# Performance work log

Hardware: AMD Instinct MI355X
Metric: run time of the kernel (lower is better)

Reference implementation:

```python
import jax, jax.numpy as jnp
import numpy as np

N_NODES = 100000
N_GRAPHS = 64

def gcn_conv(x, edge_index, W, b, num_nodes):
    # PyG GCNConv: x' = D^-1/2 (A + I) D^-1/2 (x W) + b
    h = x @ W  # [N, out]
    row, col = edge_index[0], edge_index[1]
    loops = jnp.arange(num_nodes, dtype=row.dtype)
    src = jnp.concatenate([row, loops])  # message source (x_j)
    dst = jnp.concatenate([col, loops])  # aggregation target
    deg = jax.ops.segment_sum(jnp.ones_like(src, dtype=h.dtype), dst,
                              num_segments=num_nodes)
    dinv = jnp.where(deg > 0, jax.lax.rsqrt(deg), 0.0)
    norm = dinv[src] * dinv[dst]  # [E+N]
    msgs = h[src] * norm[:, None]  # gather-transform
    out = jax.ops.segment_sum(msgs, dst, num_segments=num_nodes)  # scatter
    return out + b

def global_mean_pool(x, batch, num_graphs):
    sums = jax.ops.segment_sum(x, batch, num_segments=num_graphs)
    cnts = jax.ops.segment_sum(jnp.ones((x.shape[0],), x.dtype), batch,
                               num_segments=num_graphs)
    return sums / jnp.maximum(cnts, 1.0)[:, None]

def setup_inputs() -> dict:
    key = jax.random.key(0)
    ks = jax.random.split(key, 12)
    d_in, d_hid, d_mid, d_out = 128, 128, 20, 10
    n_edges = 1600000
    x = jax.random.normal(ks[0], (N_NODES, d_in), dtype=jnp.float32)
    edge_index = jax.random.randint(ks[1], (2, n_edges), 0, N_NODES, dtype=jnp.int64)
    batch = jnp.sort(jax.random.randint(ks[2], (N_NODES,), 0, N_GRAPHS, dtype=jnp.int64))
    def glorot(k, fan_in, fan_out):
        s = (6.0 / (fan_in + fan_out)) ** 0.5
        return jax.random.uniform(k, (fan_in, fan_out), jnp.float32, -s, s)
    return {
        "x": x, "edge_index": edge_index, "batch": batch,
        "W1": glorot(ks[3], d_in, d_hid), "b1": jnp.zeros((d_hid,), jnp.float32),
        "W2": glorot(ks[4], d_hid, d_hid), "b2": jnp.zeros((d_hid,), jnp.float32),
        "fc1_W": glorot(ks[5], d_hid, d_mid), "fc1_b": jnp.zeros((d_mid,), jnp.float32),
        "fc2_W": glorot(ks[6], d_mid, d_out), "fc2_b": jnp.zeros((d_out,), jnp.float32),
    }

def reference(x, edge_index, batch, W1, b1, W2, b2, fc1_W, fc1_b, fc2_W, fc2_b):
    # eval mode: dropout is identity
    h = gcn_conv(x, edge_index, W1, b1, N_NODES)
    h = jax.nn.elu(h)
    h = gcn_conv(h, edge_index, W2, b2, N_NODES)
    g = global_mean_pool(h, batch, N_GRAPHS)  # [G, hidden]
    g = jax.nn.relu(g @ fc1_W + fc1_b)
    g = g @ fc2_W + fc2_b
    return jax.nn.log_softmax(g, axis=1)
```

## Files before the change

kernel.cpp:

```cpp
#include <hip/hip_runtime.h>
#include <math.h>

#define DH 128
#define BCAP 16384

typedef __bf16 bf8_t __attribute__((ext_vector_type(8)));
typedef short short8 __attribute__((ext_vector_type(8)));
typedef float f4_t __attribute__((ext_vector_type(4)));
typedef float f2_t __attribute__((ext_vector_type(2)));

__device__ inline unsigned short f2b(float f) {
    unsigned int u = __builtin_bit_cast(unsigned int, f);
    u = u + 0x7fffu + ((u >> 16) & 1u);
    return (unsigned short)(u >> 16);
}
__device__ inline float b2f(unsigned short h) {
    return __builtin_bit_cast(float, (unsigned int)h << 16);
}

__global__ __launch_bounds__(256) void k_bucket(const int* __restrict__ row,
                                                const int* __restrict__ col,
                                                int E, int nbuck, int chunk,
                                                unsigned int* __restrict__ pairs,
                                                int* __restrict__ bcur) {
    __shared__ int lcnt[256];
    __shared__ int lbase[256];
    __shared__ unsigned int srec[8192];
    int t = threadIdx.x;
    int e0 = blockIdx.x * chunk;
    int e1 = min(e0 + chunk, E);
    lcnt[t] = 0;
    __syncthreads();
    for (int i = e0 + t; i < e1; i += 256) {
        int d = col[i];
        int b = d >> 9;
        int slot = atomicAdd(&lcnt[b], 1);
        srec[i - e0] = ((unsigned int)b << 22) | ((unsigned int)(d & 511) << 13)
                     | (unsigned int)slot;
    }
    __syncthreads();
    if (t < nbuck) {
        int c = lcnt[t];
        lbase[t] = (c > 0) ? atomicAdd(&bcur[t * 16], c) : 0;
    }
    __syncthreads();
    for (int i = e0 + t; i < e1; i += 256) {
        unsigned int r = srec[i - e0];
        int b = r >> 22;
        unsigned int dl = (r >> 13) & 511u;
        int slot = (int)(r & 8191u);
        int g = lbase[b] + slot;
        if (g < BCAP)
            pairs[(size_t)b * BCAP + g] = ((unsigned int)row[i] << 9) | dl;
    }
}

__global__ __launch_bounds__(256) void k_build(const unsigned int* __restrict__ pairs,
                                               const int* __restrict__ bcur,
                                               int nbuck, int N,
                                               int* __restrict__ off,
                                               int* __restrict__ dpd,
                                               float* __restrict__ dinv,
                                               int* __restrict__ csr) {
    __shared__ int cnt2[512];
    __shared__ int pd2[512];
    __shared__ int excl[512];
    __shared__ int curi[512];
    __shared__ int stmp[256];
    int b = blockIdx.x, t = threadIdx.x;
    int cnt = min(bcur[b * 16], BCAP);
    int base = b * BCAP;
    int node0 = b << 9;
    int nodes = min(512, N - node0);
    cnt2[t] = (t < nodes) ? 1 : 0;
    cnt2[t + 256] = (t + 256 < nodes) ? 1 : 0;
    __syncthreads();
    const unsigned int* pp = pairs + (size_t)b * BCAP;
    for (int i = t; i < cnt; i += 256)
        atomicAdd(&cnt2[pp[i] & 511u], 1);
    __syncthreads();
    pd2[t] = (cnt2[t] + 15) & ~15;
    pd2[t + 256] = (cnt2[t + 256] + 15) & ~15;
    __syncthreads();
    stmp[t] = pd2[2 * t] + pd2[2 * t + 1];
    __syncthreads();
    for (int d = 1; d < 256; d <<= 1) {
        int v = (t >= d) ? stmp[t - d] : 0;
        __syncthreads();
        stmp[t] += v;
        __syncthreads();
    }
    int pre = (t == 0) ? 0 : stmp[t - 1];
    excl[2 * t] = pre;
    excl[2 * t + 1] = pre + pd2[2 * t];
    __syncthreads();
    for (int n = t; n < 512; n += 256) {
        int avail = BCAP - excl[n];
        int pdc = pd2[n];
        if (pdc > avail) pdc = (avail > 0) ? (avail & ~15) : 0;
        pd2[n] = pdc;
    }
    __syncthreads();
    if (t < nodes) {
        off[node0 + t] = base + excl[t];
        dpd[node0 + t] = pd2[t];
        dinv[node0 + t] = rsqrtf((float)cnt2[t]);
    }
    int t2 = t + 256;
    if (t2 < nodes) {
        off[node0 + t2] = base + excl[t2];
        dpd[node0 + t2] = pd2[t2];
        dinv[node0 + t2] = rsqrtf((float)cnt2[t2]);
    }
    curi[t] = excl[t] + 1; curi[t + 256] = excl[t + 256] + 1;
    __syncthreads();
    for (int n = t; n < nodes; n += 256)
        if (excl[n] < BCAP) csr[base + excl[n]] = node0 + n;
    for (int i = t; i < cnt; i += 256) {
        unsigned int p = pp[i];
        int d = (int)(p & 511u);
        int slot = atomicAdd(&curi[d], 1);
        if (slot < BCAP) csr[base + slot] = (int)(p >> 9);
    }
    for (int n = t; n < 512; n += 256) {
        int e0 = excl[n] + cnt2[n];
        int e1 = excl[n] + pd2[n];
        for (int k = e0; k < e1; k++) csr[base + k] = N;
    }
}

__global__ void k_prepW(const float* __restrict__ W1, const float* __restrict__ W2,
                        unsigned short* __restrict__ Wt1, unsigned short* __restrict__ Wt2,
                        unsigned int* __restrict__ t8zrow) {
    int t = blockIdx.x * blockDim.x + threadIdx.x;
    if (blockIdx.x == 0 && threadIdx.x < 32) t8zrow[threadIdx.x] = 0u;
    int v = t & 16383;
    int k = v >> 7, n = v & 127;
    if (t < 16384) {
        Wt1[n * DH + k] = f2b(W1[k * DH + n]);
    } else {
        int p = ((k & 15) << 3) | (k >> 4);
        Wt2[n * DH + p] = f2b(W2[k * DH + n]);
    }
}

__global__ __launch_bounds__(256) void k_gemm_mfma(const void* __restrict__ Xin, int x_is_bf16,
                                                   const unsigned short* __restrict__ Wt,
                                                   const float* __restrict__ dinv,
                                                   unsigned char* __restrict__ Y, int nrows) {
    __shared__ unsigned short Xs[64 * 136];
    __shared__ unsigned short Ws[128 * 136];
    int t = threadIdx.x;
    int row0 = blockIdx.x * 64;

    for (int v = t; v < 128 * 32; v += 256) {
        int n = v >> 5, kq = v & 31;
        ushort4 w = ((const ushort4*)Wt)[v];
        *(ushort4*)&Ws[n * 136 + kq * 4] = w;
    }
    if (x_is_bf16) {
        const unsigned short* X = (const unsigned short*)Xin;
        for (int v = t; v < 64 * 32; v += 256) {
            int r = v >> 5, cq = v & 31;
            int gr = row0 + r;
            ushort4 h;
            if (gr < nrows) h = ((const ushort4*)X)[(size_t)gr * 32 + cq];
            else { h.x = 0; h.y = 0; h.z = 0; h.w = 0; }
            *(ushort4*)&Xs[r * 136 + cq * 4] = h;
        }
    } else {
        const float* X = (const float*)Xin;
        for (int v = t; v < 64 * 32; v += 256) {
            int r = v >> 5, cq = v & 31;
            int gr = row0 + r;
            ushort4 h;
            if (gr < nrows) {
                float4 xv = ((const float4*)X)[(size_t)gr * 32 + cq];
                h.x = f2b(xv.x); h.y = f2b(xv.y); h.z = f2b(xv.z); h.w = f2b(xv.w);
            } else { h.x = 0; h.y = 0; h.z = 0; h.w = 0; }
            *(ushort4*)&Xs[r * 136 + cq * 4] = h;
        }
    }
    __syncthreads();

    int w = t >> 6;
    int lane = t & 63;
    int quad = lane >> 4;
    int l16 = lane & 15;
    int rw = w * 16;

    f4_t acc[8];
#pragma unroll
    for (int j = 0; j < 8; j++) acc[j] = (f4_t){0.f, 0.f, 0.f, 0.f};

#pragma unroll
    for (int kk = 0; kk < 4; kk++) {
        int k0 = kk * 32;
        bf8_t a = __builtin_bit_cast(bf8_t,
            *(const short8*)&Xs[(rw + l16) * 136 + k0 + quad * 8]);
#pragma unroll
        for (int j = 0; j < 8; j++) {
            bf8_t b = __builtin_bit_cast(bf8_t,
                *(const short8*)&Ws[(j * 16 + l16) * 136 + k0 + quad * 8]);
            acc[j] = __builtin_amdgcn_mfma_f32_16x16x32_bf16(a, b, acc[j], 0, 0, 0);
        }
    }

#pragma unroll
    for (int reg = 0; reg < 4; reg++) {
        int r = row0 + rw + quad * 4 + reg;
        if (r < nrows) {
            float dv = dinv[r];
            float v0 = acc[0][reg] * dv, v1 = acc[1][reg] * dv;
            float v2 = acc[2][reg] * dv, v3 = acc[3][reg] * dv;
            float v4 = acc[4][reg] * dv, v5 = acc[5][reg] * dv;
            float v6 = acc[6][reg] * dv, v7 = acc[7][reg] * dv;
            int d0 = __builtin_amdgcn_cvt_pk_fp8_f32(v0, v1, 0, false);
            d0 = __builtin_amdgcn_cvt_pk_fp8_f32(v2, v3, d0, true);
            int d1 = __builtin_amdgcn_cvt_pk_fp8_f32(v4, v5, 0, false);
            d1 = __builtin_amdgcn_cvt_pk_fp8_f32(v6, v7, d1, true);
            *(uint2*)&Y[(size_t)r * DH + l16 * 8] = make_uint2((unsigned)d0, (unsigned)d1);
        }
    }
}

#define AGG_ROUND(IDX)                                                     \
    {                                                                      \
        int ea = be + i;                                                   \
        unsigned v0 = ((unsigned)IDX(ea)     << 7) | l5b;                  \
        unsigned v1 = ((unsigned)IDX(ea + 1) << 7) | l5b;                  \
        unsigned v2 = ((unsigned)IDX(ea + 2) << 7) | l5b;                  \
        unsigned v3 = ((unsigned)IDX(ea + 3) << 7) | l5b;                  \
        unsigned v4 = ((unsigned)IDX(ea + 4) << 7) | l5b;                  \
        unsigned v5 = ((unsigned)IDX(ea + 5) << 7) | l5b;                  \
        unsigned v6 = ((unsigned)IDX(ea + 6) << 7) | l5b;                  \
        unsigned v7 = ((unsigned)IDX(ea + 7) << 7) | l5b;                  \
        unsigned int u0 = *(const unsigned int*)(Tb + v0);                 \
        unsigned int u1 = *(const unsigned int*)(Tb + v1);                 \
        unsigned int u2 = *(const unsigned int*)(Tb + v2);                 \
        unsigned int u3 = *(const unsigned int*)(Tb + v3);                 \
        unsigned int u4 = *(const unsigned int*)(Tb + v4);                 \
        unsigned int u5 = *(const unsigned int*)(Tb + v5);                 \
        unsigned int u6 = *(const unsigned int*)(Tb + v6);                 \
        unsigned int u7 = *(const unsigned int*)(Tb + v7);                 \
        accA01 += __builtin_amdgcn_cvt_pk_f32_fp8(u0, false);              \
        accA23 += __builtin_amdgcn_cvt_pk_f32_fp8(u0, true);               \
        accB01 += __builtin_amdgcn_cvt_pk_f32_fp8(u1, false);              \
        accB23 += __builtin_amdgcn_cvt_pk_f32_fp8(u1, true);               \
        accA01 += __builtin_amdgcn_cvt_pk_f32_fp8(u2, false);              \
        accA23 += __builtin_amdgcn_cvt_pk_f32_fp8(u2, true);               \
        accB01 += __builtin_amdgcn_cvt_pk_f32_fp8(u3, false);              \
        accB23 += __builtin_amdgcn_cvt_pk_f32_fp8(u3, true);               \
        accA01 += __builtin_amdgcn_cvt_pk_f32_fp8(u4, false);              \
        accA23 += __builtin_amdgcn_cvt_pk_f32_fp8(u4, true);               \
        accB01 += __builtin_amdgcn_cvt_pk_f32_fp8(u5, false);              \
        accB23 += __builtin_amdgcn_cvt_pk_f32_fp8(u5, true);               \
        accA01 += __builtin_amdgcn_cvt_pk_f32_fp8(u6, false);              \
        accA23 += __builtin_amdgcn_cvt_pk_f32_fp8(u6, true);               \
        accB01 += __builtin_amdgcn_cvt_pk_f32_fp8(u7, false);              \
        accB23 += __builtin_amdgcn_cvt_pk_f32_fp8(u7, true);               \
    }

__global__ __launch_bounds__(256) void k_agg(const unsigned char* __restrict__ T,
                                             unsigned short* __restrict__ Out,
                                             const float* __restrict__ dinv,
                                             const int* __restrict__ off,
                                             const int* __restrict__ dpd,
                                             const int* __restrict__ csr,
                                             const float* __restrict__ bias,
                                             int N) {
    __shared__ int ofs[16];
    __shared__ int pds[16];
    __shared__ float dv16[16];
    __shared__ int sidx[768];
    int t = threadIdx.x;
    int d0 = blockIdx.x * 16;
    if (t < 16) {
        int n = min(d0 + t, N - 1);
        ofs[t] = off[n];
        pds[t] = dpd[n];
        dv16[t] = dinv[n];
    }
    __syncthreads();
    int s0 = ofs[0];
    int span = ofs[15] + pds[15] - s0;
    int scnt = min(span, 768);
    for (int k = t; k < scnt; k += 256) sidx[k] = csr[s0 + k];
    __syncthreads();

    int w = t >> 6;
    int lane = t & 63;
    int half = lane >> 5;
    int l5 = lane & 31;
    unsigned l5b = (unsigned)(l5 << 2);
    const char* Tb = (const char*)T;

    int c0 = ((l5 & 1) << 6) | (l5 >> 1);
    float bb0 = bias[c0], bb1 = bias[c0 + 16], bb2 = bias[c0 + 32], bb3 = bias[c0 + 48];

    for (int ni = 0; ni < 4; ni++) {
        int nl = 4 * w + ni;
        int nd = d0 + nl;
        if (nd >= N) break;
        int eL = ofs[nl] - s0;
        int pd = pds[nl];
        int K = pd >> 1;
        int be = eL + half * K;

        f2_t accA01 = (f2_t){0.f, 0.f}, accA23 = (f2_t){0.f, 0.f};
        f2_t accB01 = (f2_t){0.f, 0.f}, accB23 = (f2_t){0.f, 0.f};

        if (eL + pd <= scnt) {
#define IDX_L(e) sidx[e]
            for (int i = 0; i < K; i += 8) AGG_ROUND(IDX_L)
#undef IDX_L
        } else {
            const int* gp = csr + s0;
#define IDX_G(e) gp[e]
            for (int i = 0; i < K; i += 8) AGG_ROUND(IDX_G)
#undef IDX_G
        }

        float a0 = accA01[0] + accB01[0];
        float a1 = accA01[1] + accB01[1];
        float a2 = accA23[0] + accB23[0];
        float a3 = accA23[1] + accB23[1];
        a0 += __shfl_xor(a0, 32);
        a1 += __shfl_xor(a1, 32);
        a2 += __shfl_xor(a2, 32);
        a3 += __shfl_xor(a3, 32);

        if (!half) {
            float dv = dv16[nl];
            float o0 = a0 * dv + bb0;
            float o1 = a1 * dv + bb1;
            float o2 = a2 * dv + bb2;
            float o3 = a3 * dv + bb3;
            o0 = o0 > 0.f ? o0 : __expf(o0) - 1.f;
            o1 = o1 > 0.f ? o1 : __expf(o1) - 1.f;
            o2 = o2 > 0.f ? o2 : __expf(o2) - 1.f;
            o3 = o3 > 0.f ? o3 : __expf(o3) - 1.f;
            unsigned int p0 = (unsigned int)f2b(o0) | ((unsigned int)f2b(o1) << 16);
            unsigned int p1 = (unsigned int)f2b(o2) | ((unsigned int)f2b(o3) << 16);
            *(uint2*)&Out[(size_t)nd * DH + (l5 << 2)] = make_uint2(p0, p1);
        }
    }
}

__global__ __launch_bounds__(256) void k_aggp(const unsigned char* __restrict__ T,
                                              float* __restrict__ Gsum,
                                              const float* __restrict__ dinv,
                                              const int* __restrict__ off,
                                              const int* __restrict__ dpd,
                                              const int* __restrict__ csr,
                                              const float* __restrict__ bias,
                                              const int* __restrict__ batch,
                                              int N) {
    __shared__ int ofs[16];
    __shared__ int pds[16];
    __shared__ float dv16[16];
    __shared__ int gfs[16];
    __shared__ int sidx[768];
    __shared__ float Gacc[16 * DH];
    int t = threadIdx.x;
    int d0 = blockIdx.x * 16;
    if (t < 16) {
        int n = min(d0 + t, N - 1);
        ofs[t] = off[n];
        pds[t] = dpd[n];
        dv16[t] = dinv[n];
        gfs[t] = batch[n];
    }
    for (int k = t; k < 16 * DH; k += 256) Gacc[k] = 0.f;
    __syncthreads();
    int s0 = ofs[0];
    int g0 = gfs[0];
    int span = ofs[15] + pds[15] - s0;
    int scnt = min(span, 768);
    for (int k = t; k < scnt; k += 256) sidx[k] = csr[s0 + k];
    __syncthreads();

    int w = t >> 6;
    int lane = t & 63;
    int half = lane >> 5;
    int l5 = lane & 31;
    unsigned l5b = (unsigned)(l5 << 2);
    const char* Tb = (const char*)T;

    int c0 = ((l5 & 1) << 6) | (l5 >> 1);
    float bb0 = bias[c0], bb1 = bias[c0 + 16], bb2 = bias[c0 + 32], bb3 = bias[c0 + 48];

    for (int ni = 0; ni < 4; ni++) {
        int nl = 4 * w + ni;
        int nd = d0 + nl;
        if (nd >= N) break;
        int eL = ofs[nl] - s0;
        int pd = pds[nl];
        int K = pd >> 1;
        int be = eL + half * K;

        f2_t accA01 = (f2_t){0.f, 0.f}, accA23 = (f2_t){0.f, 0.f};
        f2_t accB01 = (f2_t){0.f, 0.f}, accB23 = (f2_t){0.f, 0.f};

        if (eL + pd <= scnt) {
#define IDX_L(e) sidx[e]
            for (int i = 0; i < K; i += 8) AGG_ROUND(IDX_L)
#undef IDX_L
        } else {
            const int* gp = csr + s0;
#define IDX_G(e) gp[e]
            for (int i = 0; i < K; i += 8) AGG_ROUND(IDX_G)
#undef IDX_G
        }

        float a0 = accA01[0] + accB01[0];
        float a1 = accA01[1] + accB01[1];
        float a2 = accA23[0] + accB23[0];
        float a3 = accA23[1] + accB23[1];
        a0 += __shfl_xor(a0, 32);
        a1 += __shfl_xor(a1, 32);
        a2 += __shfl_xor(a2, 32);
        a3 += __shfl_xor(a3, 32);

        if (!half) {
            float dv = dv16[nl];
            int sbase = (gfs[nl] - g0) * DH;
            atomicAdd(&Gacc[sbase + c0],      a0 * dv + bb0);
            atomicAdd(&Gacc[sbase + c0 + 16], a1 * dv + bb1);
            atomicAdd(&Gacc[sbase + c0 + 32], a2 * dv + bb2);
            atomicAdd(&Gacc[sbase + c0 + 48], a3 * dv + bb3);
        }
    }
    __syncthreads();
    int nspan = gfs[15] - g0 + 1;
    for (int k = t; k < nspan * DH; k += 256) {
        float v = Gacc[k];
        if (v != 0.f) atomicAdd(&Gsum[(size_t)(g0 + (k >> 7)) * DH + (k & 127)], v);
    }
}

__global__ __launch_bounds__(64) void k_head(const float* __restrict__ Gsum,
                                             const int* __restrict__ batch, int N,
                                             const float* __restrict__ W1,
                                             const float* __restrict__ b1,
                                             const float* __restrict__ W2,
                                             const float* __restrict__ b2,
                                             float* __restrict__ out) {
    int g = blockIdx.x;
    int t = threadIdx.x;
    __shared__ float gv[DH];
    __shared__ float mid[20];
    __shared__ float o[10];
    int lo = 0, hi = N;
    while (lo < hi) { int m = (lo + hi) >> 1; if (batch[m] < g) lo = m + 1; else hi = m; }
    int s = lo;
    hi = N;
    while (lo < hi) { int m = (lo + hi) >> 1; if (batch[m] < g + 1) lo = m + 1; else hi = m; }
    float inv = 1.f / fmaxf((float)(lo - s), 1.f);
    for (int i = t; i < DH; i += 64) gv[i] = Gsum[g * DH + i] * inv;
    __syncthreads();
    if (t < 20) {
        float a = b1[t];
        for (int k = 0; k < DH; k++) a += gv[k] * W1[k * 20 + t];
        mid[t] = fmaxf(a, 0.f);
    }
    __syncthreads();
    if (t < 10) {
        float a = b2[t];
        for (int k = 0; k < 20; k++) a += mid[k] * W2[k * 10 + t];
        o[t] = a;
    }
    __syncthreads();
    if (t == 0) {
        float m = -1e30f;
        for (int j = 0; j < 10; j++) m = fmaxf(m, o[j]);
        float ssum = 0.f;
        for (int j = 0; j < 10; j++) ssum += expf(o[j] - m);
        float l = logf(ssum);
        for (int j = 0; j < 10; j++) out[g * 10 + j] = o[j] - m - l;
    }
}

extern "C" void kernel_launch(void* const* d_in, const int* in_sizes, int n_in,
                              void* d_out, int out_size, void* d_ws, size_t ws_size,
                              hipStream_t stream) {
    const float* x    = (const float*)d_in[0];
    const int*   ei   = (const int*)d_in[1];
    const int*   batch= (const int*)d_in[2];
    const float* W1   = (const float*)d_in[3];
    const float* b1   = (const float*)d_in[4];
    const float* W2   = (const float*)d_in[5];
    const float* b2   = (const float*)d_in[6];
    const float* fc1W = (const float*)d_in[7];
    const float* fc1b = (const float*)d_in[8];
    const float* fc2W = (const float*)d_in[9];
    const float* fc2b = (const float*)d_in[10];
    float* out = (float*)d_out;

    int N = in_sizes[0] / DH;
    int E = in_sizes[1] / 2;
    int G = out_size / 10;
    int nbuck = (N + 511) >> 9;

    char* p = (char*)d_ws;
    auto alloc = [&](size_t bytes) {
        char* r = p;
        p += (bytes + 255) & ~(size_t)255;
        return r;
    };
    size_t pairs_bytes = (size_t)nbuck * BCAP * 4;
    size_t t8_bytes = (size_t)(N + 1) * DH;
    char* region = alloc(pairs_bytes > t8_bytes ? pairs_bytes : t8_bytes);
    unsigned int*   pairs = (unsigned int*)region;
    unsigned char*  t8    = (unsigned char*)region;
    unsigned short* a1 = (unsigned short*)alloc((size_t)N * DH * 2);
    int*   csr  = (int*)alloc((size_t)nbuck * BCAP * 4);
    int*   off  = (int*)alloc((size_t)N * 4);
    int*   dpd  = (int*)alloc((size_t)N * 4);
    float* dinv = (float*)alloc((size_t)N * 4);
    unsigned short* Wt1 = (unsigned short*)alloc(DH * DH * 2);
    unsigned short* Wt2 = (unsigned short*)alloc(DH * DH * 2);
    float* Gsum = (float*)alloc((size_t)G * DH * 4);
    int*   bcur = (int*)alloc(256 * 16 * 4);

    const int* row = ei;
    const int* col = ei + E;

    (void)hipMemsetAsync(Gsum, 0, (size_t)G * DH * 4 + 256 * 16 * 4, stream);

    const int chunk = 8192;
    int ablocks = (E + chunk - 1) / chunk;
    k_bucket<<<ablocks, 256, 0, stream>>>(row, col, E, nbuck, chunk, pairs, bcur);
    k_build<<<nbuck, 256, 0, stream>>>(pairs, bcur, nbuck, N, off, dpd, dinv, csr);
    k_prepW<<<128, 256, 0, stream>>>(W1, W2, Wt1, Wt2,
                                     (unsigned int*)(t8 + (size_t)N * DH));

    int gblocks = (N + 63) / 64;
    int mblocks = (N + 15) / 16;
    k_gemm_mfma<<<gblocks, 256, 0, stream>>>(x, 0, Wt1, dinv, t8, N);
    k_agg<<<mblocks, 256, 0, stream>>>(t8, a1, dinv, off, dpd, csr, b1, N);
    k_gemm_mfma<<<gblocks, 256, 0, stream>>>(a1, 1, Wt2, dinv, t8, N);
    k_aggp<<<mblocks, 256, 0, stream>>>(t8, Gsum, dinv, off, dpd, csr, b2, batch, N);

    k_head<<<G, 64, 0, stream>>>(Gsum, batch, N, fc1W, fc1b, fc2W, fc2b, out);
}
```

Before: 335.2 us.

## Shrink CSR buckets to 128 nodes and replace global pool atomics with partial reduction

Destination buckets drop from 512 nodes to 128 nodes with a smaller per-bucket capacity. That gives many more k_build blocks, which should parallelise CSR construction better and shorten the scans. The pooled aggregation no longer issues global atomicAdds into Gsum. Each block now writes a two-graph partial sum, and a new k_reduce kernel folds the partials per graph and divides by the node count. The cost is an extra kernel launch and tighter bucket capacity: a bucket receiving more than 4096 edges would be truncated silently.

```diff
diff --git a/kernel.cpp b/kernel.cpp
--- a/kernel.cpp
+++ b/kernel.cpp
@@ -2,7 +2,7 @@
 #include <math.h>
 
 #define DH 128
-#define BCAP 16384
+#define BCAP 4096
 
 typedef __bf16 bf8_t __attribute__((ext_vector_type(8)));
 typedef short short8 __attribute__((ext_vector_type(8)));
@@ -23,35 +23,35 @@
                                                 int E, int nbuck, int chunk,
                                                 unsigned int* __restrict__ pairs,
                                                 int* __restrict__ bcur) {
-    __shared__ int lcnt[256];
-    __shared__ int lbase[256];
-    __shared__ unsigned int srec[8192];
+    __shared__ int lcnt[800];
+    __shared__ int lbase[800];
+    __shared__ unsigned int srec[2048];
     int t = threadIdx.x;
     int e0 = blockIdx.x * chunk;
     int e1 = min(e0 + chunk, E);
-    lcnt[t] = 0;
+    for (int i = t; i < nbuck; i += 256) lcnt[i] = 0;
     __syncthreads();
     for (int i = e0 + t; i < e1; i += 256) {
         int d = col[i];
-        int b = d >> 9;
+        int b = d >> 7;
         int slot = atomicAdd(&lcnt[b], 1);
-        srec[i - e0] = ((unsigned int)b << 22) | ((unsigned int)(d & 511) << 13)
+        srec[i - e0] = ((unsigned int)b << 19) | ((unsigned int)(d & 127) << 12)
                      | (unsigned int)slot;
     }
     __syncthreads();
-    if (t < nbuck) {
-        int c = lcnt[t];
-        lbase[t] = (c > 0) ? atomicAdd(&bcur[t * 16], c) : 0;
+    for (int bb = t; bb < nbuck; bb += 256) {
+        int c = lcnt[bb];
+        lbase[bb] = (c > 0) ? atomicAdd(&bcur[bb * 16], c) : 0;
     }
     __syncthreads();
     for (int i = e0 + t; i < e1; i += 256) {
         unsigned int r = srec[i - e0];
-        int b = r >> 22;
-        unsigned int dl = (r >> 13) & 511u;
-        int slot = (int)(r & 8191u);
+        int b = r >> 19;
+        unsigned int dl = (r >> 12) & 127u;
+        int slot = (int)(r & 4095u);
         int g = lbase[b] + slot;
         if (g < BCAP)
-            pairs[(size_t)b * BCAP + g] = ((unsigned int)row[i] << 9) | dl;
+            pairs[(size_t)b * BCAP + g] = ((unsigned int)row[i] << 7) | dl;
     }
 }
 
@@ -62,70 +62,49 @@
                                                int* __restrict__ dpd,
                                                float* __restrict__ dinv,
                                                int* __restrict__ csr) {
-    __shared__ int cnt2[512];
-    __shared__ int pd2[512];
-    __shared__ int excl[512];
-    __shared__ int curi[512];
-    __shared__ int stmp[256];
+    __shared__ int cnt2[128];
+    __shared__ int pd2[128];
+    __shared__ int curi[128];
+    __shared__ int scn[128];
     int b = blockIdx.x, t = threadIdx.x;
     int cnt = min(bcur[b * 16], BCAP);
     int base = b * BCAP;
-    int node0 = b << 9;
-    int nodes = min(512, N - node0);
-    cnt2[t] = (t < nodes) ? 1 : 0;
-    cnt2[t + 256] = (t + 256 < nodes) ? 1 : 0;
+    int node0 = b << 7;
+    int nodes = min(128, N - node0);
+    if (t < 128) cnt2[t] = (t < nodes) ? 1 : 0;
     __syncthreads();
     const unsigned int* pp = pairs + (size_t)b * BCAP;
     for (int i = t; i < cnt; i += 256)
-        atomicAdd(&cnt2[pp[i] & 511u], 1);
-    __syncthreads();
-    pd2[t] = (cnt2[t] + 15) & ~15;
-    pd2[t + 256] = (cnt2[t + 256] + 15) & ~15;
-    __syncthreads();
-    stmp[t] = pd2[2 * t] + pd2[2 * t + 1];
-    __syncthreads();
-    for (int d = 1; d < 256; d <<= 1) {
-        int v = (t >= d) ? stmp[t - d] : 0;
+        atomicAdd(&cnt2[pp[i] & 127u], 1);
+    __syncthreads();
+    if (t < 128) { int pdv = (cnt2[t] + 15) & ~15; pd2[t] = pdv; scn[t] = pdv; }
+    __syncthreads();
+    for (int d = 1; d < 128; d <<= 1) {
+        int v = (t < 128 && t >= d) ? scn[t - d] : 0;
         __syncthreads();
-        stmp[t] += v;
+        if (t < 128) scn[t] += v;
         __syncthreads();
     }
-    int pre = (t == 0) ? 0 : stmp[t - 1];
-    excl[2 * t] = pre;
-    excl[2 * t + 1] = pre + pd2[2 * t];
-    __syncthreads();
-    for (int n = t; n < 512; n += 256) {
-        int avail = BCAP - excl[n];
-        int pdc = pd2[n];
-        if (pdc > avail) pdc = (avail > 0) ? (avail & ~15) : 0;
-        pd2[n] = pdc;
-    }
-    __syncthreads();
-    if (t < nodes) {
-        off[node0 + t] = base + excl[t];
-        dpd[node0 + t] = pd2[t];
-        dinv[node0 + t] = rsqrtf((float)cnt2[t]);
-    }
-    int t2 = t + 256;
-    if (t2 < nodes) {
-        off[node0 + t2] = base + excl[t2];
-        dpd[node0 + t2] = pd2[t2];
-        dinv[node0 + t2] = rsqrtf((float)cnt2[t2]);
-    }
-    curi[t] = excl[t] + 1; curi[t + 256] = excl[t + 256] + 1;
-    __syncthreads();
-    for (int n = t; n < nodes; n += 256)
-        if (excl[n] < BCAP) csr[base + excl[n]] = node0 + n;
+    if (t < 128) {
+        int pdv = pd2[t];
+        int exc = min(scn[t] - pdv, BCAP);
+        int avail = BCAP - exc;
+        int pdc = min(pdv, avail);
+        curi[t] = exc + 1;
+        if (t < nodes) {
+            off[node0 + t] = base + exc;
+            dpd[node0 + t] = pdc;
+            dinv[node0 + t] = rsqrtf((float)cnt2[t]);
+            if (pdc > 0) csr[base + exc] = node0 + t;
+            for (int k = cnt2[t]; k < pdc; k++) csr[base + exc + k] = N;
+        }
+    }
+    __syncthreads();
     for (int i = t; i < cnt; i += 256) {
         unsigned int p = pp[i];
-        int d = (int)(p & 511u);
+        int d = (int)(p & 127u);
         int slot = atomicAdd(&curi[d], 1);
-        if (slot < BCAP) csr[base + slot] = (int)(p >> 9);
-    }
-    for (int n = t; n < 512; n += 256) {
-        int e0 = excl[n] + cnt2[n];
-        int e1 = excl[n] + pd2[n];
-        for (int k = e0; k < e1; k++) csr[base + k] = N;
+        if (slot < BCAP) csr[base + slot] = (int)(p >> 7);
     }
 }
 
@@ -347,8 +326,9 @@
     }
 }
 
-__global__ __launch_bounds__(256) void k_aggp(const unsigned char* __restrict__ T,
-                                              float* __restrict__ Gsum,
+__global__ __launch_bounds__(256) void k_agg2(const unsigned char* __restrict__ T,
+                                              float* __restrict__ partials,
+                                              int* __restrict__ pg0,
                                               const float* __restrict__ dinv,
                                               const int* __restrict__ off,
                                               const int* __restrict__ dpd,
@@ -361,7 +341,7 @@
     __shared__ float dv16[16];
     __shared__ int gfs[16];
     __shared__ int sidx[768];
-    __shared__ float Gacc[16 * DH];
+    __shared__ float Gacc[256];
     int t = threadIdx.x;
     int d0 = blockIdx.x * 16;
     if (t < 16) {
@@ -371,7 +351,7 @@
         dv16[t] = dinv[n];
         gfs[t] = batch[n];
     }
-    for (int k = t; k < 16 * DH; k += 256) Gacc[k] = 0.f;
+    Gacc[t] = 0.f;
     __syncthreads();
     int s0 = ofs[0];
     int g0 = gfs[0];
@@ -424,23 +404,41 @@
 
         if (!half) {
             float dv = dv16[nl];
-            int sbase = (gfs[nl] - g0) * DH;
-            atomicAdd(&Gacc[sbase + c0],      a0 * dv + bb0);
-            atomicAdd(&Gacc[sbase + c0 + 16], a1 * dv + bb1);
-            atomicAdd(&Gacc[sbase + c0 + 32], a2 * dv + bb2);
-            atomicAdd(&Gacc[sbase + c0 + 48], a3 * dv + bb3);
-        }
-    }
-    __syncthreads();
-    int nspan = gfs[15] - g0 + 1;
-    for (int k = t; k < nspan * DH; k += 256) {
-        float v = Gacc[k];
-        if (v != 0.f) atomicAdd(&Gsum[(size_t)(g0 + (k >> 7)) * DH + (k & 127)], v);
-    }
+            int sb = min(gfs[nl] - g0, 1) << 7;
+            atomicAdd(&Gacc[sb + c0],      a0 * dv + bb0);
+            atomicAdd(&Gacc[sb + c0 + 16], a1 * dv + bb1);
+            atomicAdd(&Gacc[sb + c0 + 32], a2 * dv + bb2);
+            atomicAdd(&Gacc[sb + c0 + 48], a3 * dv + bb3);
+        }
+    }
+    __syncthreads();
+    partials[(size_t)blockIdx.x * 256 + t] = Gacc[t];
+    if (t == 0) pg0[blockIdx.x] = g0;
+}
+
+__global__ __launch_bounds__(128) void k_reduce(const float* __restrict__ partials,
+                                                const int* __restrict__ pg0,
+                                                const int* __restrict__ batch,
+                                                int N, float* __restrict__ Gsum) {
+    int g = blockIdx.x;
+    int t = threadIdx.x;
+    int lo = 0, hi = N;
+    while (lo < hi) { int m = (lo + hi) >> 1; if (batch[m] < g) lo = m + 1; else hi = m; }
+    int s = lo;
+    hi = N;
+    while (lo < hi) { int m = (lo + hi) >> 1; if (batch[m] < g + 1) lo = m + 1; else hi = m; }
+    int e = lo;
+    int b0 = s >> 4;
+    int b1 = (e - 1) >> 4;
+    float a = 0.f;
+    for (int b = b0; b <= b1; b++) {
+        int d = g - pg0[b];
+        if (d >= 0 && d <= 1) a += partials[(size_t)b * 256 + (d << 7) + t];
+    }
+    Gsum[g * DH + t] = a / fmaxf((float)(e - s), 1.f);
 }
 
 __global__ __launch_bounds__(64) void k_head(const float* __restrict__ Gsum,
-                                             const int* __restrict__ batch, int N,
                                              const float* __restrict__ W1,
                                              const float* __restrict__ b1,
                                              const float* __restrict__ W2,
@@ -451,13 +449,7 @@
     __shared__ float gv[DH];
     __shared__ float mid[20];
     __shared__ float o[10];
-    int lo = 0, hi = N;
-    while (lo < hi) { int m = (lo + hi) >> 1; if (batch[m] < g) lo = m + 1; else hi = m; }
-    int s = lo;
-    hi = N;
-    while (lo < hi) { int m = (lo + hi) >> 1; if (batch[m] < g + 1) lo = m + 1; else hi = m; }
-    float inv = 1.f / fmaxf((float)(lo - s), 1.f);
-    for (int i = t; i < DH; i += 64) gv[i] = Gsum[g * DH + i] * inv;
+    for (int i = t; i < DH; i += 64) gv[i] = Gsum[g * DH + i];
     __syncthreads();
     if (t < 20) {
         float a = b1[t];
@@ -500,7 +492,8 @@
     int N = in_sizes[0] / DH;
     int E = in_sizes[1] / 2;
     int G = out_size / 10;
-    int nbuck = (N + 511) >> 9;
+    int nbuck = (N + 127) >> 7;
+    int mblocks = (N + 15) / 16;
 
     char* p = (char*)d_ws;
     auto alloc = [&](size_t bytes) {
@@ -518,17 +511,19 @@
     int*   off  = (int*)alloc((size_t)N * 4);
     int*   dpd  = (int*)alloc((size_t)N * 4);
     float* dinv = (float*)alloc((size_t)N * 4);
+    float* partials = (float*)alloc((size_t)mblocks * 256 * 4);
+    int*   pg0  = (int*)alloc((size_t)mblocks * 4);
     unsigned short* Wt1 = (unsigned short*)alloc(DH * DH * 2);
     unsigned short* Wt2 = (unsigned short*)alloc(DH * DH * 2);
     float* Gsum = (float*)alloc((size_t)G * DH * 4);
-    int*   bcur = (int*)alloc(256 * 16 * 4);
+    int*   bcur = (int*)alloc(800 * 16 * 4);
 
     const int* row = ei;
     const int* col = ei + E;
 
-    (void)hipMemsetAsync(Gsum, 0, (size_t)G * DH * 4 + 256 * 16 * 4, stream);
-
-    const int chunk = 8192;
+    (void)hipMemsetAsync(bcur, 0, 800 * 16 * 4, stream);
+
+    const int chunk = 2048;
     int ablocks = (E + chunk - 1) / chunk;
     k_bucket<<<ablocks, 256, 0, stream>>>(row, col, E, nbuck, chunk, pairs, bcur);
     k_build<<<nbuck, 256, 0, stream>>>(pairs, bcur, nbuck, N, off, dpd, dinv, csr);
@@ -536,11 +531,11 @@
                                      (unsigned int*)(t8 + (size_t)N * DH));
 
     int gblocks = (N + 63) / 64;
-    int mblocks = (N + 15) / 16;
     k_gemm_mfma<<<gblocks, 256, 0, stream>>>(x, 0, Wt1, dinv, t8, N);
     k_agg<<<mblocks, 256, 0, stream>>>(t8, a1, dinv, off, dpd, csr, b1, N);
     k_gemm_mfma<<<gblocks, 256, 0, stream>>>(a1, 1, Wt2, dinv, t8, N);
-    k_aggp<<<mblocks, 256, 0, stream>>>(t8, Gsum, dinv, off, dpd, csr, b2, batch, N);
-
-    k_head<<<G, 64, 0, stream>>>(Gsum, batch, N, fc1W, fc1b, fc2W, fc2b, out);
-}
+    k_agg2<<<mblocks, 256, 0, stream>>>(t8, partials, pg0, dinv, off, dpd, csr, b2, batch, N);
+
+    k_reduce<<<G, 128, 0, stream>>>(partials, pg0, batch, N, Gsum);
+    k_head<<<G, 64, 0, stream>>>(Gsum, fc1W, fc1b, fc2W, fc2b, out);
+}
```

New measurement: 388.1 us. +15.8%, slower.
